# Optimization experiments

Hardware: AMD Instinct MI355X
Metric: run time of the kernel (lower is better)

The kernel has to match this reference:

```python
import jax, jax.numpy as jnp
import numpy as np

K_CODES = 1024
D_DIM = 256


def setup_inputs() -> dict:
    key = jax.random.key(0)
    k1, k2 = jax.random.split(key)
    z_e_x = jax.random.normal(k1, (64, D_DIM, 32, 32), dtype=jnp.float32)
    # codebook init uniform(-1/K, 1/K) as in the torch module
    emb = jax.random.uniform(k2, (K_CODES, D_DIM), dtype=jnp.float32,
                             minval=-1.0 / K_CODES, maxval=1.0 / K_CODES)
    return {"z_e_x": z_e_x, "emb": emb}


def _nearest_indices(z_flat, emb):
    # z_flat: [N, D], emb: [K, D] -> [N] argmin_k ||z - e_k||^2
    # expand ||z-e||^2 = ||z||^2 - 2 z.e + ||e||^2 (GEMM-dominated)
    d = (jnp.sum(z_flat * z_flat, axis=-1, keepdims=True)
         - 2.0 * (z_flat @ emb.T)
         + jnp.sum(emb * emb, axis=-1))  # [N, K]
    return jnp.argmin(d, axis=-1)


def reference(z_e_x, emb):
    # Faithful to VQEmbedding.forward: permute NCHW->NHWC, vq() -> indices [B,H,W]
    B, D, H, W = z_e_x.shape
    z = jnp.transpose(z_e_x, (0, 2, 3, 1)).reshape(-1, D)  # [B*H*W, D]
    idx = _nearest_indices(z, emb)
    return idx.reshape(B, H, W)
```

## Files before the change

### kernel.cpp

```cpp
#include <hip/hip_runtime.h>
#include <float.h>
#include <stdint.h>

#define K_CODES 1024
#define D_DIM   256
#define NPTS    65536
#define K2      512
#define CAP     32
#define DELTA   2e-3f

using short8  = __attribute__((ext_vector_type(8))) short;
using float4v = __attribute__((ext_vector_type(4))) float;

#define A2_OFF     ((size_t)0)
#define A2_BYTES   ((size_t)NPTS * K2 * 2)
#define B2_OFF     (A2_OFF + A2_BYTES)
#define B2_BYTES   ((size_t)K_CODES * K2 * 2)
#define EN_OFF     (B2_OFF + B2_BYTES)
#define EN_BYTES   ((size_t)K_CODES * 4)
#define ZN_OFF     (EN_OFF + EN_BYTES)
#define ZN_BYTES   ((size_t)NPTS * 4)
#define CNT_OFF    (ZN_OFF + ZN_BYTES)
#define CNT_BYTES  ((size_t)NPTS * 4)
#define CAND_OFF   (CNT_OFF + CNT_BYTES)
#define CAND_BYTES ((size_t)NPTS * CAP * 4)
#define WS_NEED    (CAND_OFF + CAND_BYTES)

#define FB_EN_OFF 0
#define FB_ZN_OFF ((size_t)K_CODES * 4)

__device__ __forceinline__ uint16_t f2bf(float x) {
    uint32_t u = __float_as_uint(x);
    return (uint16_t)((u + 0x7FFFu + ((u >> 16) & 1u)) >> 16);
}
__device__ __forceinline__ float bf2f(uint16_t h) {
    return __uint_as_float(((uint32_t)h) << 16);
}
__device__ __forceinline__ unsigned enc_f(float f) {
    unsigned u = __float_as_uint(f);
    return (u & 0x80000000u) ? ~u : (u | 0x80000000u);
}
__device__ __forceinline__ float dec_f(unsigned u) {
    unsigned v = (u & 0x80000000u) ? (u & 0x7FFFFFFFu) : ~u;
    return __uint_as_float(v);
}
__device__ __forceinline__ void gl_lds16(const void* g, void* l) {
    __builtin_amdgcn_global_load_lds(
        (const __attribute__((address_space(1))) void*)g,
        (__attribute__((address_space(3))) void*)l, 16, 0, 0);
}

__global__ __launch_bounds__(256) void znorm_kernel(const float* __restrict__ z,
                                                    float* __restrict__ znorm) {
#pragma clang fp contract(off) reassociate(off)
    const int n = blockIdx.x * 256 + threadIdx.x;
    const int b = n >> 10, hw = n & 1023;
    const float* zp = z + (size_t)b * (D_DIM * 1024) + hw;
    float tot0, tot1;
    {
        float r[8];
#pragma unroll
        for (int j = 0; j < 8; ++j) { float x = zp[(size_t)j * 1024]; r[j] = x * x; }
        for (int i = 1; i < 16; ++i) {
#pragma unroll
            for (int j = 0; j < 8; ++j) {
                float x = zp[(size_t)(8 * i + j) * 1024];
                r[j] = r[j] + x * x;
            }
        }
        tot0 = ((r[0] + r[1]) + (r[2] + r[3])) + ((r[4] + r[5]) + (r[6] + r[7]));
    }
    {
        const float* zq = zp + (size_t)128 * 1024;
        float r[8];
#pragma unroll
        for (int j = 0; j < 8; ++j) { float x = zq[(size_t)j * 1024]; r[j] = x * x; }
        for (int i = 1; i < 16; ++i) {
#pragma unroll
            for (int j = 0; j < 8; ++j) {
                float x = zq[(size_t)(8 * i + j) * 1024];
                r[j] = r[j] + x * x;
            }
        }
        tot1 = ((r[0] + r[1]) + (r[2] + r[3])) + ((r[4] + r[5]) + (r[6] + r[7]));
    }
    znorm[n] = tot0 + tot1;
}

__global__ __launch_bounds__(256) void enorm_kernel(const float* __restrict__ emb,
                                                    float* __restrict__ enorm) {
#pragma clang fp contract(off) reassociate(off)
    const int c = blockIdx.x * 256 + threadIdx.x;
    const float* e = emb + (size_t)c * D_DIM;
    float tot0, tot1;
    {
        float r[8];
#pragma unroll
        for (int j = 0; j < 8; ++j) { float x = e[j]; r[j] = x * x; }
        for (int i = 1; i < 16; ++i) {
#pragma unroll
            for (int j = 0; j < 8; ++j) { float x = e[8 * i + j]; r[j] = r[j] + x * x; }
        }
        tot0 = ((r[0] + r[1]) + (r[2] + r[3])) + ((r[4] + r[5]) + (r[6] + r[7]));
    }
    {
        const float* e2 = e + 128;
        float r[8];
#pragma unroll
        for (int j = 0; j < 8; ++j) { float x = e2[j]; r[j] = x * x; }
        for (int i = 1; i < 16; ++i) {
#pragma unroll
            for (int j = 0; j < 8; ++j) { float x = e2[8 * i + j]; r[j] = r[j] + x * x; }
        }
        tot1 = ((r[0] + r[1]) + (r[2] + r[3])) + ((r[4] + r[5]) + (r[6] + r[7]));
    }
    enorm[c] = tot0 + tot1;
}

__global__ __launch_bounds__(256) void conv_e_kernel(const float* __restrict__ emb,
                                                     uint16_t* __restrict__ B2) {
    const int c = blockIdx.x, d = threadIdx.x;
    float x = emb[(size_t)c * D_DIM + d];
    uint16_t h = f2bf(x);
    uint16_t l = f2bf(x - bf2f(h));
    B2[(size_t)c * K2 + d]         = h;
    B2[(size_t)c * K2 + 256 + d]   = l;
}

__global__ __launch_bounds__(256) void conv_z_kernel(const float* __restrict__ z,
                                                     uint16_t* __restrict__ A2) {
    __shared__ float ld[64 * 65];
    const int t = threadIdx.x;
    const int pb = blockIdx.x;
    const int b = pb >> 4, hw0 = (pb & 15) << 6;
    const float* zb = z + (size_t)b * (D_DIM * 1024) + hw0;
    const int w = t >> 6, p = t & 63;
    const int p2 = t >> 2, qq = t & 3;

    for (int dt = 0; dt < 4; ++dt) {
        __syncthreads();
#pragma unroll
        for (int r = 0; r < 16; ++r) {
            int dl = w + 4 * r;
            ld[dl * 65 + p] = zb[(size_t)(dt * 64 + dl) * 1024 + p];
        }
        __syncthreads();
        uint16_t hs[16], ls[16];
#pragma unroll
        for (int i = 0; i < 16; ++i) {
            float v = ld[(qq * 16 + i) * 65 + p2];
            uint16_t h = f2bf(v);
            hs[i] = h;
            ls[i] = f2bf(v - bf2f(h));
        }
        size_t nbase = (size_t)(pb * 64 + p2) * K2 + dt * 64 + qq * 16;
#pragma unroll
        for (int g = 0; g < 4; ++g) {
            *(ushort4*)&A2[nbase + 4 * g] =
                make_ushort4(hs[4 * g], hs[4 * g + 1], hs[4 * g + 2], hs[4 * g + 3]);
            *(ushort4*)&A2[nbase + 256 + 4 * g] =
                make_ushort4(ls[4 * g], ls[4 * g + 1], ls[4 * g + 2], ls[4 * g + 3]);
        }
    }
}

__global__ __launch_bounds__(256) void vq_mfma_kernel(const uint16_t* __restrict__ A2,
                                                      const uint16_t* __restrict__ B2,
                                                      const float* __restrict__ enorm,
                                                      unsigned* __restrict__ cnt,
                                                      unsigned* __restrict__ cand) {
    __shared__ short As[64 * 64];
    __shared__ short Bs[256 * 64];
    __shared__ unsigned pmin[64];

    const int t    = threadIdx.x;
    const int w    = t >> 6;
    const int ln   = t & 63;
    const int quad = ln >> 4;
    const int col  = ln & 15;
    const int l3   = ln >> 3, l7 = ln & 7;
    const int pb   = blockIdx.x;

    if (t < 64) pmin[t] = 0xFFFFFFFFu;

    const int arow = pb * 64 + w * 16 + l3;

    for (int ct = 0; ct < 4; ++ct) {
        float4v s[4][4];
#pragma unroll
        for (int i = 0; i < 4; ++i)
#pragma unroll
            for (int j = 0; j < 4; ++j) s[i][j] = (float4v)0.0f;

        for (int chunk = 0; chunk < 8; ++chunk) {
            const int k0 = chunk * 64;
            __syncthreads();
#pragma unroll
            for (int i = 0; i < 2; ++i) {
                gl_lds16(A2 + (size_t)(arow + i * 8) * K2 + k0 + l7 * 8,
                         &As[w * 1024 + i * 512]);
            }
#pragma unroll
            for (int i = 0; i < 8; ++i) {
                int c = ct * 256 + w * 64 + i * 8 + l3;
                gl_lds16(B2 + (size_t)c * K2 + k0 + l7 * 8,
                         &Bs[w * 4096 + i * 512]);
            }
            __syncthreads();
#pragma unroll
            for (int kh = 0; kh < 2; ++kh) {
                const int kk = kh * 32 + quad * 8;
                short8 a[4], bfr[4];
#pragma unroll
                for (int tm = 0; tm < 4; ++tm)
                    a[tm] = *(const short8*)&As[(tm * 16 + col) * 64 + kk];
#pragma unroll
                for (int tn = 0; tn < 4; ++tn)
                    bfr[tn] = *(const short8*)&Bs[(w * 64 + tn * 16 + col) * 64 + kk];
#pragma unroll
                for (int tm = 0; tm < 4; ++tm)
#pragma unroll
                    for (int tn = 0; tn < 4; ++tn)
                        s[tm][tn] = __builtin_amdgcn_mfma_f32_16x16x32_bf16(
                            a[tm], bfr[tn], s[tm][tn], 0, 0, 0);
            }
        }
        float en4[4];
#pragma unroll
        for (int tn = 0; tn < 4; ++tn)
            en4[tn] = enorm[ct * 256 + w * 64 + tn * 16 + col];
#pragma unroll
        for (int tm = 0; tm < 4; ++tm)
#pragma unroll
            for (int tn = 0; tn < 4; ++tn)
#pragma unroll
                for (int r = 0; r < 4; ++r)
                    s[tm][tn][r] = en4[tn] - 2.0f * s[tm][tn][r];
#pragma unroll
        for (int tm = 0; tm < 4; ++tm)
#pragma unroll
            for (int r = 0; r < 4; ++r) {
                float v = fminf(fminf(s[tm][0][r], s[tm][1][r]),
                                fminf(s[tm][2][r], s[tm][3][r]));
                atomicMin(&pmin[tm * 16 + quad * 4 + r], enc_f(v));
            }
        __syncthreads();
#pragma unroll
        for (int tm = 0; tm < 4; ++tm)
#pragma unroll
            for (int r = 0; r < 4; ++r) {
                const int m = tm * 16 + quad * 4 + r;
                const float thr = dec_f(pmin[m]) + DELTA;
                const unsigned n = pb * 64 + m;
#pragma unroll
                for (int tn = 0; tn < 4; ++tn) {
                    if (s[tm][tn][r] <= thr) {
                        unsigned c = ct * 256 + w * 64 + tn * 16 + col;
                        unsigned idx = atomicAdd(&cnt[n], 1u);
                        if (idx < CAP) cand[(size_t)n * CAP + idx] = c;
                    }
                }
            }
    }
}

__global__ __launch_bounds__(256) void rescore_kernel(const float* __restrict__ z,
                                                      const float* __restrict__ emb,
                                                      const float* __restrict__ enorm,
                                                      const float* __restrict__ znorm,
                                                      const unsigned* __restrict__ cnt,
                                                      const unsigned* __restrict__ cand,
                                                      int* __restrict__ out) {
    const int n = blockIdx.x * 256 + threadIdx.x;
    const int b = n >> 10, hw = n & 1023;
    const float* zp = z + (size_t)b * (D_DIM * 1024) + hw;
    int k = (int)cnt[n];
    if (k > CAP) k = CAP;
    if (k < 1) k = 1;
    const float zn = znorm[n];
    float bv = FLT_MAX;
    int   bi = 0x7FFFFFFF;
    for (int g0 = 0; g0 < k; g0 += 4) {
        int gk = k - g0; if (gk > 4) gk = 4;
        int cs[4];
        float dot[4];
#pragma unroll
        for (int j = 0; j < 4; ++j) { dot[j] = 0.f; cs[j] = 0; }
        for (int j = 0; j < gk; ++j) cs[j] = (int)cand[(size_t)n * CAP + g0 + j];
        for (int d = 0; d < D_DIM; ++d) {
            float zv = zp[(size_t)d * 1024];
#pragma unroll
            for (int j = 0; j < 4; ++j)
                dot[j] = __builtin_fmaf(zv, emb[(size_t)cs[j] * D_DIM + d], dot[j]);
        }
        {
#pragma clang fp contract(off) reassociate(off)
            for (int j = 0; j < gk; ++j) {
                float t1 = zn - 2.0f * dot[j];
                float sc = t1 + enorm[cs[j]];
                if (sc < bv || (sc == bv && cs[j] < bi)) { bv = sc; bi = cs[j]; }
            }
        }
    }
    out[n] = bi;
}

#define PT 64
#define CT 256
#define DC 32
__global__ __launch_bounds__(256) void vq_kernel(const float* __restrict__ z,
                                                 const float* __restrict__ emb,
                                                 const float* __restrict__ enorm,
                                                 const float* __restrict__ znorm,
                                                 int* __restrict__ out) {
    __shared__ float zc[DC * PT];
    __shared__ float ec[DC * CT];
    __shared__ float redv[PT * 17];
    __shared__ int   redi[PT * 17];
    const int t  = threadIdx.x;
    const int pg = t >> 4;
    const int cg = t & 15;
    const int pb = blockIdx.x;
    const int b  = pb >> 4;
    const int hw0 = (pb & 15) << 6;
    const float* zbase = z + (size_t)b * (D_DIM * 1024) + hw0;
    float zn[4];
#pragma unroll
    for (int i = 0; i < 4; ++i) zn[i] = znorm[pb * PT + 4 * pg + i];
    float best_v[4]; int best_i[4];
#pragma unroll
    for (int i = 0; i < 4; ++i) { best_v[i] = FLT_MAX; best_i[i] = 0; }
    for (int tile = 0; tile < K_CODES / CT; ++tile) {
        float acc[4][16];
#pragma unroll
        for (int i = 0; i < 4; ++i)
#pragma unroll
            for (int j = 0; j < 16; ++j) acc[i][j] = 0.f;
        for (int chunk = 0; chunk < D_DIM / DC; ++chunk) {
            const int d0 = chunk * DC;
            __syncthreads();
            {
                int p = t & 63, dp = t >> 6;
#pragma unroll
                for (int r = 0; r < 8; ++r) {
                    int d = 4 * r + dp;
                    zc[d * PT + p] = zbase[(size_t)(d0 + d) * 1024 + p];
                }
            }
            {
                int q = t & 7, cr = t >> 3;
#pragma unroll
                for (int r = 0; r < 8; ++r) {
                    int cl = 32 * r + cr;
                    int c  = tile * CT + cl;
                    float4 v = *(const float4*)(emb + (size_t)c * D_DIM + d0 + 4 * q);
                    int dd = 4 * q;
                    ec[(dd + 0) * CT + cl] = v.x;
                    ec[(dd + 1) * CT + cl] = v.y;
                    ec[(dd + 2) * CT + cl] = v.z;
                    ec[(dd + 3) * CT + cl] = v.w;
                }
            }
            __syncthreads();
#pragma unroll 4
            for (int d = 0; d < DC; ++d) {
                float4 zf = *(const float4*)&zc[d * PT + 4 * pg];
                float4 ef[4];
#pragma unroll
                for (int j = 0; j < 4; ++j)
                    ef[j] = *(const float4*)&ec[d * CT + 64 * j + 4 * cg];
                const float zz[4] = { zf.x, zf.y, zf.z, zf.w };
#pragma unroll
                for (int i = 0; i < 4; ++i) {
                    float zi = zz[i];
#pragma unroll
                    for (int j = 0; j < 4; ++j) {
                        acc[i][4 * j + 0] += zi * ef[j].x;
                        acc[i][4 * j + 1] += zi * ef[j].y;
                        acc[i][4 * j + 2] += zi * ef[j].z;
                        acc[i][4 * j + 3] += zi * ef[j].w;
                    }
                }
            }
        }
        {
#pragma clang fp contract(off) reassociate(off)
#pragma unroll
            for (int j = 0; j < 4; ++j) {
#pragma unroll
                for (int jj = 0; jj < 4; ++jj) {
                    int c = tile * CT + 64 * j + 4 * cg + jj;
                    float en = enorm[c];
#pragma unroll
                    for (int i = 0; i < 4; ++i) {
                        float t1 = zn[i] - 2.0f * acc[i][4 * j + jj];
                        float sc = t1 + en;
                        if (sc < best_v[i] || (sc == best_v[i] && c < best_i[i])) {
                            best_v[i] = sc; best_i[i] = c;
                        }
                    }
                }
            }
        }
    }
#pragma unroll
    for (int i = 0; i < 4; ++i) {
        int p = 4 * pg + i;
        redv[p * 17 + cg] = best_v[i];
        redi[p * 17 + cg] = best_i[i];
    }
    __syncthreads();
    if (t < PT) {
        float bv = FLT_MAX; int bi = 0;
        for (int g = 0; g < 16; ++g) {
            float v = redv[t * 17 + g];
            int  ix = redi[t * 17 + g];
            if (v < bv || (v == bv && ix < bi)) { bv = v; bi = ix; }
        }
        out[pb * PT + t] = bi;
    }
}

extern "C" void kernel_launch(void* const* d_in, const int* in_sizes, int n_in,
                              void* d_out, int out_size, void* d_ws, size_t ws_size,
                              hipStream_t stream) {
    const float* z   = (const float*)d_in[0];
    const float* emb = (const float*)d_in[1];
    int* out = (int*)d_out;
    char* ws = (char*)d_ws;

    if (ws_size >= WS_NEED) {
        uint16_t* A2    = (uint16_t*)(ws + A2_OFF);
        uint16_t* B2    = (uint16_t*)(ws + B2_OFF);
        float*    en    = (float*)(ws + EN_OFF);
        float*    zn    = (float*)(ws + ZN_OFF);
        unsigned* cnt   = (unsigned*)(ws + CNT_OFF);
        unsigned* cand  = (unsigned*)(ws + CAND_OFF);

        hipMemsetAsync(cnt, 0, CNT_BYTES, stream);
        conv_e_kernel<<<K_CODES, 256, 0, stream>>>(emb, B2);
        conv_z_kernel<<<NPTS / 64, 256, 0, stream>>>(z, A2);
        enorm_kernel<<<K_CODES / 256, 256, 0, stream>>>(emb, en);
        znorm_kernel<<<NPTS / 256, 256, 0, stream>>>(z, zn);
        vq_mfma_kernel<<<NPTS / 64, 256, 0, stream>>>(A2, B2, en, cnt, cand);
        rescore_kernel<<<NPTS / 256, 256, 0, stream>>>(z, emb, en, zn, cnt, cand, out);
    } else {
        float* en = (float*)(ws + FB_EN_OFF);
        float* zn = (float*)(ws + FB_ZN_OFF);
        enorm_kernel<<<K_CODES / 256, 256, 0, stream>>>(emb, en);
        znorm_kernel<<<NPTS / 256, 256, 0, stream>>>(z, zn);
        vq_kernel<<<NPTS / PT, 256, 0, stream>>>(z, emb, en, zn, out);
    }
}
```

Baseline: 387.7 us.

## Fuse prep kernels, swizzle LDS tiles, and vectorize rescore loads

Merges codebook bf16 split conversion with norm computation into one kernel. Zeroing the candidate counters moves into the z conversion kernel, and the z norm is computed inside rescore, which drops the memset and two launches. Adds an XOR swizzle to the LDS layout of the MFMA tiles to cut bank conflicts. Changes the conv_z store pattern and vectorizes the rescore dot products with float4 codebook loads. In exchange, rescore now reads z twice and prep_e uses only 4 blocks, so parallelism there is low.

```diff
diff --git a/kernel.cpp b/kernel.cpp
--- a/kernel.cpp
+++ b/kernel.cpp
@@ -117,18 +117,43 @@
     enorm[c] = tot0 + tot1;
 }
 
-__global__ __launch_bounds__(256) void conv_e_kernel(const float* __restrict__ emb,
-                                                     uint16_t* __restrict__ B2) {
-    const int c = blockIdx.x, d = threadIdx.x;
-    float x = emb[(size_t)c * D_DIM + d];
-    uint16_t h = f2bf(x);
-    uint16_t l = f2bf(x - bf2f(h));
-    B2[(size_t)c * K2 + d]         = h;
-    B2[(size_t)c * K2 + 256 + d]   = l;
+__global__ __launch_bounds__(256) void prep_e_kernel(const float* __restrict__ emb,
+                                                     uint16_t* __restrict__ B2,
+                                                     float* __restrict__ enorm) {
+#pragma clang fp contract(off) reassociate(off)
+    const int c = blockIdx.x * 256 + threadIdx.x;
+    const float* e = emb + (size_t)c * D_DIM;
+    uint16_t* Bp = B2 + (size_t)c * K2;
+    float tot[2];
+#pragma unroll
+    for (int half = 0; half < 2; ++half) {
+        const float* eh = e + 128 * half;
+        float r[8];
+        for (int i = 0; i < 16; ++i) {
+            uint16_t hs[8], ls[8];
+#pragma unroll
+            for (int j = 0; j < 8; ++j) {
+                float x = eh[8 * i + j];
+                uint16_t h = f2bf(x);
+                hs[j] = h;
+                ls[j] = f2bf(x - bf2f(h));
+                float sq = x * x;
+                if (i == 0) r[j] = sq; else r[j] = r[j] + sq;
+            }
+            int d = half * 128 + 8 * i;
+            *(ushort4*)&Bp[d]           = make_ushort4(hs[0], hs[1], hs[2], hs[3]);
+            *(ushort4*)&Bp[d + 4]       = make_ushort4(hs[4], hs[5], hs[6], hs[7]);
+            *(ushort4*)&Bp[256 + d]     = make_ushort4(ls[0], ls[1], ls[2], ls[3]);
+            *(ushort4*)&Bp[256 + d + 4] = make_ushort4(ls[4], ls[5], ls[6], ls[7]);
+        }
+        tot[half] = ((r[0] + r[1]) + (r[2] + r[3])) + ((r[4] + r[5]) + (r[6] + r[7]));
+    }
+    enorm[c] = tot[0] + tot[1];
 }
 
 __global__ __launch_bounds__(256) void conv_z_kernel(const float* __restrict__ z,
-                                                     uint16_t* __restrict__ A2) {
+                                                     uint16_t* __restrict__ A2,
+                                                     unsigned* __restrict__ cnt) {
     __shared__ float ld[64 * 65];
     const int t = threadIdx.x;
     const int pb = blockIdx.x;
@@ -137,6 +162,8 @@
     const int w = t >> 6, p = t & 63;
     const int p2 = t >> 2, qq = t & 3;
 
+    if (t < 64) cnt[pb * 64 + t] = 0;
+
     for (int dt = 0; dt < 4; ++dt) {
         __syncthreads();
 #pragma unroll
@@ -145,21 +172,21 @@
             ld[dl * 65 + p] = zb[(size_t)(dt * 64 + dl) * 1024 + p];
         }
         __syncthreads();
-        uint16_t hs[16], ls[16];
-#pragma unroll
-        for (int i = 0; i < 16; ++i) {
-            float v = ld[(qq * 16 + i) * 65 + p2];
-            uint16_t h = f2bf(v);
-            hs[i] = h;
-            ls[i] = f2bf(v - bf2f(h));
-        }
-        size_t nbase = (size_t)(pb * 64 + p2) * K2 + dt * 64 + qq * 16;
-#pragma unroll
-        for (int g = 0; g < 4; ++g) {
-            *(ushort4*)&A2[nbase + 4 * g] =
-                make_ushort4(hs[4 * g], hs[4 * g + 1], hs[4 * g + 2], hs[4 * g + 3]);
-            *(ushort4*)&A2[nbase + 256 + 4 * g] =
-                make_ushort4(ls[4 * g], ls[4 * g + 1], ls[4 * g + 2], ls[4 * g + 3]);
+        size_t nb = (size_t)(pb * 64 + p2) * K2 + dt * 64;
+#pragma unroll
+        for (int i = 0; i < 4; ++i) {
+            uint16_t hs[4], ls[4];
+#pragma unroll
+            for (int m = 0; m < 4; ++m) {
+                float v = ld[(i * 16 + qq * 4 + m) * 65 + p2];
+                uint16_t h = f2bf(v);
+                hs[m] = h;
+                ls[m] = f2bf(v - bf2f(h));
+            }
+            *(ushort4*)&A2[nb + i * 16 + qq * 4] =
+                make_ushort4(hs[0], hs[1], hs[2], hs[3]);
+            *(ushort4*)&A2[nb + 256 + i * 16 + qq * 4] =
+                make_ushort4(ls[0], ls[1], ls[2], ls[3]);
         }
     }
 }
@@ -184,6 +211,8 @@
     if (t < 64) pmin[t] = 0xFFFFFFFFu;
 
     const int arow = pb * 64 + w * 16 + l3;
+    const int ksw  = (l7 ^ l3) * 8;
+    const int csw  = (col & 7);
 
     for (int ct = 0; ct < 4; ++ct) {
         float4v s[4][4];
@@ -197,26 +226,26 @@
             __syncthreads();
 #pragma unroll
             for (int i = 0; i < 2; ++i) {
-                gl_lds16(A2 + (size_t)(arow + i * 8) * K2 + k0 + l7 * 8,
+                gl_lds16(A2 + (size_t)(arow + i * 8) * K2 + k0 + ksw,
                          &As[w * 1024 + i * 512]);
             }
 #pragma unroll
             for (int i = 0; i < 8; ++i) {
                 int c = ct * 256 + w * 64 + i * 8 + l3;
-                gl_lds16(B2 + (size_t)c * K2 + k0 + l7 * 8,
+                gl_lds16(B2 + (size_t)c * K2 + k0 + ksw,
                          &Bs[w * 4096 + i * 512]);
             }
             __syncthreads();
 #pragma unroll
             for (int kh = 0; kh < 2; ++kh) {
-                const int kk = kh * 32 + quad * 8;
+                const int kg = ((kh * 4 + quad) ^ csw) * 8;
                 short8 a[4], bfr[4];
 #pragma unroll
                 for (int tm = 0; tm < 4; ++tm)
-                    a[tm] = *(const short8*)&As[(tm * 16 + col) * 64 + kk];
+                    a[tm] = *(const short8*)&As[(tm * 16 + col) * 64 + kg];
 #pragma unroll
                 for (int tn = 0; tn < 4; ++tn)
-                    bfr[tn] = *(const short8*)&Bs[(w * 64 + tn * 16 + col) * 64 + kk];
+                    bfr[tn] = *(const short8*)&Bs[(w * 64 + tn * 16 + col) * 64 + kg];
 #pragma unroll
                 for (int tm = 0; tm < 4; ++tm)
 #pragma unroll
@@ -267,17 +296,50 @@
 __global__ __launch_bounds__(256) void rescore_kernel(const float* __restrict__ z,
                                                       const float* __restrict__ emb,
                                                       const float* __restrict__ enorm,
-                                                      const float* __restrict__ znorm,
                                                       const unsigned* __restrict__ cnt,
                                                       const unsigned* __restrict__ cand,
                                                       int* __restrict__ out) {
     const int n = blockIdx.x * 256 + threadIdx.x;
     const int b = n >> 10, hw = n & 1023;
     const float* zp = z + (size_t)b * (D_DIM * 1024) + hw;
+
+    float zn;
+    {
+#pragma clang fp contract(off) reassociate(off)
+        float tot0, tot1;
+        {
+            float r[8];
+#pragma unroll
+            for (int j = 0; j < 8; ++j) { float x = zp[(size_t)j * 1024]; r[j] = x * x; }
+            for (int i = 1; i < 16; ++i) {
+#pragma unroll
+                for (int j = 0; j < 8; ++j) {
+                    float x = zp[(size_t)(8 * i + j) * 1024];
+                    r[j] = r[j] + x * x;
+                }
+            }
+            tot0 = ((r[0] + r[1]) + (r[2] + r[3])) + ((r[4] + r[5]) + (r[6] + r[7]));
+        }
+        {
+            const float* zq = zp + (size_t)128 * 1024;
+            float r[8];
+#pragma unroll
+            for (int j = 0; j < 8; ++j) { float x = zq[(size_t)j * 1024]; r[j] = x * x; }
+            for (int i = 1; i < 16; ++i) {
+#pragma unroll
+                for (int j = 0; j < 8; ++j) {
+                    float x = zq[(size_t)(8 * i + j) * 1024];
+                    r[j] = r[j] + x * x;
+                }
+            }
+            tot1 = ((r[0] + r[1]) + (r[2] + r[3])) + ((r[4] + r[5]) + (r[6] + r[7]));
+        }
+        zn = tot0 + tot1;
+    }
+
     int k = (int)cnt[n];
     if (k > CAP) k = CAP;
     if (k < 1) k = 1;
-    const float zn = znorm[n];
     float bv = FLT_MAX;
     int   bi = 0x7FFFFFFF;
     for (int g0 = 0; g0 < k; g0 += 4) {
@@ -285,13 +347,37 @@
         int cs[4];
         float dot[4];
 #pragma unroll
-        for (int j = 0; j < 4; ++j) { dot[j] = 0.f; cs[j] = 0; }
-        for (int j = 0; j < gk; ++j) cs[j] = (int)cand[(size_t)n * CAP + g0 + j];
-        for (int d = 0; d < D_DIM; ++d) {
-            float zv = zp[(size_t)d * 1024];
-#pragma unroll
-            for (int j = 0; j < 4; ++j)
-                dot[j] = __builtin_fmaf(zv, emb[(size_t)cs[j] * D_DIM + d], dot[j]);
+        for (int j = 0; j < 4; ++j) {
+            cs[j] = (int)cand[(size_t)n * CAP + g0 + (j < gk ? j : 0)];
+            dot[j] = 0.f;
+        }
+        for (int d0 = 0; d0 < D_DIM; d0 += 16) {
+            float zv[16];
+#pragma unroll
+            for (int m = 0; m < 16; ++m) zv[m] = zp[(size_t)(d0 + m) * 1024];
+#pragma unroll
+            for (int j = 0; j < 4; ++j) {
+                const float4* er = (const float4*)(emb + (size_t)cs[j] * D_DIM + d0);
+                float4 e0 = er[0], e1 = er[1], e2 = er[2], e3 = er[3];
+                float dj = dot[j];
+                dj = __builtin_fmaf(zv[0],  e0.x, dj);
+                dj = __builtin_fmaf(zv[1],  e0.y, dj);
+                dj = __builtin_fmaf(zv[2],  e0.z, dj);
+                dj = __builtin_fmaf(zv[3],  e0.w, dj);
+                dj = __builtin_fmaf(zv[4],  e1.x, dj);
+                dj = __builtin_fmaf(zv[5],  e1.y, dj);
+                dj = __builtin_fmaf(zv[6],  e1.z, dj);
+                dj = __builtin_fmaf(zv[7],  e1.w, dj);
+                dj = __builtin_fmaf(zv[8],  e2.x, dj);
+                dj = __builtin_fmaf(zv[9],  e2.y, dj);
+                dj = __builtin_fmaf(zv[10], e2.z, dj);
+                dj = __builtin_fmaf(zv[11], e2.w, dj);
+                dj = __builtin_fmaf(zv[12], e3.x, dj);
+                dj = __builtin_fmaf(zv[13], e3.y, dj);
+                dj = __builtin_fmaf(zv[14], e3.z, dj);
+                dj = __builtin_fmaf(zv[15], e3.w, dj);
+                dot[j] = dj;
+            }
         }
         {
 #pragma clang fp contract(off) reassociate(off)
@@ -433,22 +519,18 @@
         uint16_t* A2    = (uint16_t*)(ws + A2_OFF);
         uint16_t* B2    = (uint16_t*)(ws + B2_OFF);
         float*    en    = (float*)(ws + EN_OFF);
-        float*    zn    = (float*)(ws + ZN_OFF);
         unsigned* cnt   = (unsigned*)(ws + CNT_OFF);
         unsigned* cand  = (unsigned*)(ws + CAND_OFF);
 
-        hipMemsetAsync(cnt, 0, CNT_BYTES, stream);
-        conv_e_kernel<<<K_CODES, 256, 0, stream>>>(emb, B2);
-        conv_z_kernel<<<NPTS / 64, 256, 0, stream>>>(z, A2);
-        enorm_kernel<<<K_CODES / 256, 256, 0, stream>>>(emb, en);
-        znorm_kernel<<<NPTS / 256, 256, 0, stream>>>(z, zn);
+        prep_e_kernel<<<K_CODES / 256, 256, 0, stream>>>(emb, B2, en);
+        conv_z_kernel<<<NPTS / 64, 256, 0, stream>>>(z, A2, cnt);
         vq_mfma_kernel<<<NPTS / 64, 256, 0, stream>>>(A2, B2, en, cnt, cand);
-        rescore_kernel<<<NPTS / 256, 256, 0, stream>>>(z, emb, en, zn, cnt, cand, out);
+        rescore_kernel<<<NPTS / 256, 256, 0, stream>>>(z, emb, en, cnt, cand, out);
     } else {
-        float* en = (float*)(ws + FB_EN_OFF);
-        float* zn = (float*)(ws + FB_ZN_OFF);
-        enorm_kernel<<<K_CODES / 256, 256, 0, stream>>>(emb, en);
-        znorm_kernel<<<NPTS / 256, 256, 0, stream>>>(z, zn);
-        vq_kernel<<<NPTS / PT, 256, 0, stream>>>(z, emb, en, zn, out);
-    }
-}
+        float* enf = (float*)(ws + FB_EN_OFF);
+        float* znf = (float*)(ws + FB_ZN_OFF);
+        enorm_kernel<<<K_CODES / 256, 256, 0, stream>>>(emb, enf);
+        znorm_kernel<<<NPTS / 256, 256, 0, stream>>>(z, znf);
+        vq_kernel<<<NPTS / PT, 256, 0, stream>>>(z, emb, enf, znf, out);
+    }
+}
```

After: 391.6 us. About the same (+1.0%).
